# Kernel optimization log

Measured on AMD Instinct MI355X. Metric: run time of the kernel, lower is better.

The kernel has to match this reference:

```python
import jax, jax.numpy as jnp
import numpy as np
import math

N_EMB = 256
N_HEAD = 8
B_SEGS = 128
T_SEG = 256  # equal-length segments; N = B_SEGS * T_SEG


def setup_inputs() -> dict:
    key = jax.random.key(0)
    ks = jax.random.split(key, 10)
    N = B_SEGS * T_SEG
    x = jax.random.normal(ks[0], (N, N_EMB), dtype=jnp.float32)
    batch = jnp.repeat(jnp.arange(B_SEGS, dtype=jnp.int64), T_SEG)
    s = 1.0 / math.sqrt(N_EMB)
    def lin(k):
        kw, kb = jax.random.split(k)
        W = jax.random.uniform(kw, (N_EMB, N_EMB), jnp.float32, -s, s)
        b = jax.random.uniform(kb, (N_EMB,), jnp.float32, -s, s)
        return W, b
    Wq, bq = lin(ks[1])
    Wk, bk = lin(ks[2])
    Wv, bv = lin(ks[3])
    Wp, bp = lin(ks[4])
    return {"x": x, "batch": batch, "Wq": Wq, "bq": bq, "Wk": Wk, "bk": bk,
            "Wv": Wv, "bv": bv, "Wp": Wp, "bp": bp}


def reference(x, batch, Wq, bq, Wk, bk, Wv, bv, Wp, bp):
    # Dropout layers are identity in eval / p=0.
    N, C = x.shape
    H = N_HEAD
    hd = C // H
    B = int(batch[-1]) + 1        # equal-length segments
    T = N // B
    xr = x.reshape(B, T, C)
    # per-segment QKV projections: [B,H,T,hd]
    def heads(W, b):
        return (xr @ W.T + b).reshape(B, T, H, hd).transpose(0, 2, 1, 3)
    q = heads(Wq, bq)
    k = heads(Wk, bk)
    v = heads(Wv, bv)
    scores = jnp.einsum('bhtd,bhsd->bhts', q, k) * (1.0 / math.sqrt(hd))
    attn = jax.nn.softmax(scores, axis=-1)          # [B,H,T,T]
    y = jnp.einsum('bhts,bhsd->bhtd', attn, v)      # [B,H,T,hd]
    y = y.transpose(0, 2, 1, 3).reshape(B, T, C)
    y = y @ Wp.T + bp
    attn_mean = attn.mean(axis=1)                   # head-mean per segment [B,T,T]
    return y.reshape(N, C), attn_mean
```

## Files before the change

### kernel.cpp

```cpp
#include <hip/hip_runtime.h>
#include <hip/hip_bf16.h>
#include <stdint.h>

typedef unsigned short u16;
typedef __bf16 bf16_t;
typedef bf16_t bf16x8 __attribute__((ext_vector_type(8)));
typedef float f32x4 __attribute__((ext_vector_type(4)));

#define NTOK 32768
#define CEMB 256
#define NHEAD 8
#define HD 32
#define BSEG 128
#define TSEG 256

#define SCQ (0.17677669529663687f * 1.4426950408889634f)

static __device__ __forceinline__ bf16x8 ld16(const u16* p) {
  uint4 v = *reinterpret_cast<const uint4*>(p);
  return __builtin_bit_cast(bf16x8, v);
}
static __device__ __forceinline__ u16 f2b(float f) {
  return __builtin_bit_cast(u16, (bf16_t)f);
}
static __device__ __forceinline__ uint4 cvt8(float4 a, float4 b) {
  u16 o[8] = {f2b(a.x), f2b(a.y), f2b(a.z), f2b(a.w),
              f2b(b.x), f2b(b.y), f2b(b.z), f2b(b.w)};
  return *reinterpret_cast<const uint4*>(o);
}

typedef __attribute__((address_space(1))) const void GASV;
typedef __attribute__((address_space(3))) void LASV;
static __device__ __forceinline__ void stage16(const u16* g, u16* l) {
  __builtin_amdgcn_global_load_lds((GASV*)g, (LASV*)l, 16, 0, 0);
}

__global__ __launch_bounds__(1024, 4)
void k_qkv(const float* __restrict__ x,
           const float* __restrict__ Wq, const float* __restrict__ Wk,
           const float* __restrict__ Wv,
           const float* __restrict__ bq, const float* __restrict__ bk,
           const float* __restrict__ bv,
           u16* __restrict__ q_ws, u16* __restrict__ k_ws, u16* __restrict__ v_ws) {
  const int d = blockIdx.x;
  const int m_idx = (d & 7) * 32 + (d >> 3);
  const int m0 = m_idx * 128;
  const int tid = threadIdx.x;
  const int w = tid >> 6, l = tid & 63;
  const int lr = l & 15, lg = l >> 4;
  const int wrP = w >> 2, wcP = w & 3;

  extern __shared__ char lds[];
  char* bounce = lds + 131072;

  const int brow = tid >> 2;
  const int bcb = (tid & 3) * 2;
  float4 breg[2][4];
  auto BLOAD = [&](int bi, float4* r4) {
    const float* Wsel = (bi >> 2) == 0 ? Wq : ((bi >> 2) == 1 ? Wk : Wv);
    const float* s = Wsel + (size_t)brow * CEMB + (bi & 3) * 64 + bcb * 8;
    r4[0] = reinterpret_cast<const float4*>(s)[0];
    r4[1] = reinterpret_cast<const float4*>(s)[1];
    r4[2] = reinterpret_cast<const float4*>(s)[2];
    r4[3] = reinterpret_cast<const float4*>(s)[3];
  };
  auto BWRITE = [&](const float4* r4, int par) {
    char* Bs = lds + 65536 + par * 32768;
#pragma unroll
    for (int jj = 0; jj < 2; ++jj) {
      int byte = brow * 128 + (((bcb + jj) * 16) ^ ((brow & 7) << 4));
      *reinterpret_cast<uint4*>(Bs + byte) = cvt8(r4[jj * 2], r4[jj * 2 + 1]);
    }
  };

  BLOAD(0, breg[0]);
  {
    int row = tid >> 3, seg = tid & 7;
    const float* src = x + (size_t)(m0 + row) * CEMB + seg * 32;
#pragma unroll
    for (int j = 0; j < 4; ++j) {
      float4 a = reinterpret_cast<const float4*>(src)[2 * j];
      float4 b = reinterpret_cast<const float4*>(src)[2 * j + 1];
      int byte = row * 512 + ((seg * 64 + j * 16) ^ ((row & 7) << 4));
      *reinterpret_cast<uint4*>(lds + byte) = cvt8(a, b);
    }
  }
  BWRITE(breg[0], 0);
  BLOAD(1, breg[1]);
  __syncthreads();

#pragma unroll
  for (int mode = 0; mode < 3; ++mode) {
    f32x4 acc[2][4];
#pragma unroll
    for (int mf = 0; mf < 2; ++mf)
#pragma unroll
      for (int nf = 0; nf < 4; ++nf) {
        f32x4 z = {0.f, 0.f, 0.f, 0.f};
        acc[mf][nf] = z;
      }

#pragma unroll
    for (int kt = 0; kt < 4; ++kt) {
      const int bi = mode * 4 + kt;
      const int par = bi & 1;
      if (bi < 11) BWRITE(breg[(bi + 1) & 1], (bi + 1) & 1);
      if (bi < 10) BLOAD(bi + 2, breg[bi & 1]);
      const char* Bs = lds + 65536 + par * 32768;
      bf16x8 av[2][2], bw[4][2];
#pragma unroll
      for (int mf = 0; mf < 2; ++mf)
#pragma unroll
        for (int kk = 0; kk < 2; ++kk) {
          int row = wrP * 32 + mf * 16 + lr;
          int byte = row * 512 + ((kt * 128 + kk * 64 + lg * 16) ^ ((row & 7) << 4));
          av[mf][kk] = *reinterpret_cast<const bf16x8*>(lds + byte);
        }
#pragma unroll
      for (int nf = 0; nf < 4; ++nf)
#pragma unroll
        for (int kk = 0; kk < 2; ++kk) {
          int row = wcP * 64 + nf * 16 + lr;
          int byte = row * 128 + ((kk * 64 + lg * 16) ^ ((row & 7) << 4));
          bw[nf][kk] = *reinterpret_cast<const bf16x8*>(Bs + byte);
        }
#pragma unroll
      for (int kk = 0; kk < 2; ++kk)
#pragma unroll
        for (int nf = 0; nf < 4; ++nf)
#pragma unroll
          for (int mf = 0; mf < 2; ++mf)
            acc[mf][nf] = __builtin_amdgcn_mfma_f32_16x16x32_bf16(
                av[mf][kk], bw[nf][kk], acc[mf][nf], 0, 0, 0);
      __syncthreads();
    }

    const float* bias = (mode == 0) ? bq : ((mode == 1) ? bk : bv);
    float bb[4];
#pragma unroll
    for (int nf = 0; nf < 4; ++nf) bb[nf] = bias[wcP * 64 + nf * 16 + lr];

    if (mode < 2) {
      const float osc = (mode == 0) ? SCQ : 1.0f;
      u16* outp = (mode == 0) ? q_ws : k_ws;
#pragma unroll
      for (int g = 0; g < 2; ++g) {
        if ((wrP >> 1) == g) {
#pragma unroll
          for (int mf = 0; mf < 2; ++mf)
#pragma unroll
            for (int nf = 0; nf < 4; ++nf)
#pragma unroll
              for (int r = 0; r < 4; ++r) {
                int lrow = (wrP & 1) * 32 + mf * 16 + lg * 4 + r;
                int col = wcP * 64 + nf * 16 + lr;
                int byte = lrow * 512 + ((col * 2) ^ ((lrow & 7) << 4));
                *(u16*)(bounce + byte) = f2b((acc[mf][nf][r] + bb[nf]) * osc);
              }
        }
        __syncthreads();
#pragma unroll
        for (int jj = 0; jj < 2; ++jj) {
          int ch = tid * 2 + jj;
          int crow = ch >> 5, cc = ch & 31;
          int byte = crow * 512 + ((cc * 16) ^ ((crow & 7) << 4));
          *reinterpret_cast<uint4*>(outp + (size_t)(m0 + g * 64 + crow) * CEMB + cc * 8) =
              *reinterpret_cast<const uint4*>(bounce + byte);
        }
        __syncthreads();
      }
    } else {
      const int bs = m0 >> 8, t0 = m0 & 255;
#pragma unroll
      for (int g = 0; g < 2; ++g) {
        if ((wcP >> 1) == g) {
#pragma unroll
          for (int mf = 0; mf < 2; ++mf)
#pragma unroll
            for (int nf = 0; nf < 4; ++nf)
#pragma unroll
              for (int r = 0; r < 4; ++r) {
                int row = wrP * 32 + mf * 16 + lg * 4 + r;
                int ccol = (wcP & 1) * 64 + nf * 16 + lr;
                int byte = ccol * 256 + ((row * 2) ^ ((ccol & 7) << 4));
                *(u16*)(bounce + byte) = f2b(acc[mf][nf][r] + bb[nf]);
              }
        }
        __syncthreads();
#pragma unroll
        for (int jj = 0; jj < 2; ++jj) {
          int ch = tid * 2 + jj;
          int ccl = ch >> 4, cc = ch & 15;
          int byte = ccl * 256 + ((cc * 16) ^ ((ccl & 7) << 4));
          int c = g * 128 + ccl, hh = c >> 5, dd = c & 31;
          *reinterpret_cast<uint4*>(
              v_ws + ((size_t)(bs * NHEAD + hh) * HD + dd) * TSEG + t0 + cc * 8) =
              *reinterpret_cast<const uint4*>(bounce + byte);
        }
        __syncthreads();
      }
    }
  }
}

__global__ __launch_bounds__(1024, 4)
void k_attn(const u16* __restrict__ q_ws, const u16* __restrict__ k_ws,
            const u16* __restrict__ v_ws, const float* __restrict__ Wp,
            const float* __restrict__ bp,
            float* __restrict__ out, float* __restrict__ mean_out) {
  const int dblk = blockIdx.x;
  const int xcd = dblk & 7, ii = dblk >> 3;
  const int b = xcd * 16 + (ii >> 1);
  const int th = ii & 1;
  const int tid = threadIdx.x;
  const int w = tid >> 6, l = tid & 63;
  const int lr = l & 15, lg = l >> 4;
  const int wt = w & 7, sh = w >> 3;
  const int tbase = th * 128 + wt * 16;

  extern __shared__ u16 ldsKV[];
  float* smb = reinterpret_cast<float*>(ldsKV + 32768);
  float* ylds = reinterpret_cast<float*>(ldsKV + 33280);
  char* yTile = reinterpret_cast<char*>(ldsKV) + 83968;

  float macc[8][4];
#pragma unroll
  for (int st = 0; st < 8; ++st)
#pragma unroll
    for (int r = 0; r < 4; ++r) macc[st][r] = 0.f;

  const u16* qseg = q_ws + (size_t)b * TSEG * CEMB;
  const u16* kseg = k_ws + (size_t)b * TSEG * CEMB;
  const u16* vseg = v_ws + (size_t)(b * NHEAD) * HD * TSEG;

  auto STAGE_KV = [&](int hn, int bn) {
    int idx = tid;
    int c = idx >> 6, l2 = idx & 63;
    int lr2 = l2 & 15, lg2 = l2 >> 4;
    int srow = 32 * (c >> 1) + 4 * (c & 1) + 8 * (lr2 >> 2) + (lr2 & 3);
    stage16(kseg + srow * CEMB + hn * HD + lg2 * 8, ldsKV + (bn * 1024 + idx) * 8);
    int vrow = (c >> 3) * 16 + lr2;
    int vcol = (c & 7) * 32 + lg2 * 8;
    stage16(vseg + (size_t)(hn * HD + vrow) * TSEG + vcol,
            ldsKV + 16384 + (bn * 1024 + idx) * 8);
  };

  STAGE_KV(0, 0);
  bf16x8 qf = ld16(qseg + (tbase + lr) * CEMB + lg * 8);

  const int own_slot = wt * 2 + sh;
  const int par_slot = wt * 2 + (1 - sh);

  for (int h = 0; h < NHEAD; ++h) {
    const int bn = h & 1;
    __syncthreads();
    if (h < 7) STAGE_KV(h + 1, bn ^ 1);
    const u16* Kb = ldsKV + bn * 8192;
    const u16* Vb = ldsKV + 16384 + bn * 8192;

    float s[8][4];
    __builtin_amdgcn_s_setprio(1);
#pragma unroll
    for (int st = 0; st < 8; ++st) {
      bf16x8 kf = *reinterpret_cast<const bf16x8*>(Kb + ((sh * 8 + st) * 64 + l) * 8);
      f32x4 z = {0.f, 0.f, 0.f, 0.f};
      f32x4 dd = __builtin_amdgcn_mfma_f32_16x16x32_bf16(kf, qf, z, 0, 0, 0);
#pragma unroll
      for (int r = 0; r < 4; ++r) s[st][r] = dd[r];
    }
    __builtin_amdgcn_s_setprio(0);

    qf = ld16(qseg + (tbase + lr) * CEMB + ((h + 1) & 7) * HD + lg * 8);

    float s0 = 0.f, s1 = 0.f, s2 = 0.f, s3 = 0.f;
#pragma unroll
    for (int st = 0; st < 8; ++st) {
      float p0 = exp2f(s[st][0]);
      float p1 = exp2f(s[st][1]);
      float p2 = exp2f(s[st][2]);
      float p3 = exp2f(s[st][3]);
      s[st][0] = p0; s[st][1] = p1; s[st][2] = p2; s[st][3] = p3;
      s0 += p0; s1 += p1; s2 += p2; s3 += p3;
    }
    float sm = (s0 + s1) + (s2 + s3);
    sm += __shfl_xor(sm, 16, 64);
    sm += __shfl_xor(sm, 32, 64);

    bf16x8 pb[4];
#pragma unroll
    for (int kk = 0; kk < 4; ++kk)
#pragma unroll
      for (int e = 0; e < 4; ++e) {
        pb[kk][e] = (bf16_t)s[2 * kk][e];
        pb[kk][4 + e] = (bf16_t)s[2 * kk + 1][e];
      }

    f32x4 y0 = {0.f, 0.f, 0.f, 0.f}, y1 = {0.f, 0.f, 0.f, 0.f};
    __builtin_amdgcn_s_setprio(1);
#pragma unroll
    for (int kk = 0; kk < 4; ++kk) {
      bf16x8 vf0 = *reinterpret_cast<const bf16x8*>(Vb + ((0 * 8 + sh * 4 + kk) * 64 + l) * 8);
      bf16x8 vf1 = *reinterpret_cast<const bf16x8*>(Vb + ((1 * 8 + sh * 4 + kk) * 64 + l) * 8);
      y0 = __builtin_amdgcn_mfma_f32_16x16x32_bf16(vf0, pb[kk], y0, 0, 0, 0);
      y1 = __builtin_amdgcn_mfma_f32_16x16x32_bf16(vf1, pb[kk], y1, 0, 0, 0);
    }
    __builtin_amdgcn_s_setprio(0);

    if (l < 16) smb[own_slot * 16 + l] = sm;
    {
      f32x4 ywr = (sh == 0) ? y1 : y0;
      *reinterpret_cast<f32x4*>(ylds + own_slot * 272 + lg * 68 + lr * 4) = ywr;
    }

    __builtin_amdgcn_sched_barrier(0);
    asm volatile("s_waitcnt lgkmcnt(0)" ::: "memory");
    __builtin_amdgcn_s_barrier();
    __builtin_amdgcn_sched_barrier(0);

    float smT = sm + smb[par_slot * 16 + lr];
    float inv = __builtin_amdgcn_rcpf(smT);

#pragma unroll
    for (int st = 0; st < 8; ++st)
#pragma unroll
      for (int r = 0; r < 4; ++r)
        macc[st][r] = fmaf(s[st][r], inv, macc[st][r]);

    {
      f32x4 ymine = (sh == 0) ? y0 : y1;
      f32x4 ypar = *reinterpret_cast<const f32x4*>(ylds + par_slot * 272 + lg * 68 + lr * 4);
      u16 o[4];
#pragma unroll
      for (int r = 0; r < 4; ++r) o[r] = f2b((ymine[r] + ypar[r]) * inv);
      int row = wt * 16 + lr;
      int colb = h * 64 + sh * 32 + lg * 8;
      *reinterpret_cast<uint2*>(yTile + row * 512 + (colb ^ ((row & 7) << 4))) =
          *reinterpret_cast<const uint2*>(o);
    }
  }

  __syncthreads();

  const int wrow = tid >> 2;
  const int wcb = (tid & 3) * 2;
  float4 wreg[2][4];
  auto WLOAD = [&](int kt, float4* r4) {
    const float* s = Wp + (size_t)wrow * CEMB + kt * 64 + wcb * 8;
    r4[0] = reinterpret_cast<const float4*>(s)[0];
    r4[1] = reinterpret_cast<const float4*>(s)[1];
    r4[2] = reinterpret_cast<const float4*>(s)[2];
    r4[3] = reinterpret_cast<const float4*>(s)[3];
  };
  auto WWRITE = [&](const float4* r4, int bn) {
#pragma unroll
    for (int jj = 0; jj < 2; ++jj) {
      int byte = bn * 32768 + wrow * 128 + (((wcb + jj) * 16) ^ ((wrow & 7) << 4));
      *reinterpret_cast<uint4*>(reinterpret_cast<char*>(ldsKV) + byte) =
          cvt8(r4[jj * 2], r4[jj * 2 + 1]);
    }
  };

  WLOAD(0, wreg[0]);

  {
    float* smem = reinterpret_cast<float*>(ldsKV);
    float* smw = smem + w * (16 * 65) + lr * 65;
    const int trow = l >> 2;
    const int cql = (l & 3) * 4;
    const float* srcp = smem + w * (16 * 65) + trow * 65 + cql;
    float* gdst = mean_out + (size_t)(b * TSEG + tbase + trow) * TSEG + sh * 128 + cql;
    for (int c = 0; c < 2; ++c) {
#pragma unroll
      for (int j = 0; j < 4; ++j) {
        int st = 4 * c + j;
        int sl = 32 * ((st >> 1) & 1) + 4 * (st & 1) + 8 * lg;
#pragma unroll
        for (int r = 0; r < 4; ++r) smw[sl + r] = macc[st][r] * 0.125f;
      }
#pragma unroll
      for (int j = 0; j < 4; ++j)
        *reinterpret_cast<f32x4*>(gdst + c * 64 + j * 16) =
            *reinterpret_cast<const f32x4*>(srcp + j * 16);
    }
  }
  __syncthreads();

  {
    const int wrP = w >> 2, wcP = w & 3;

    WWRITE(wreg[0], 0);
    WLOAD(1, wreg[1]);
    __syncthreads();

    f32x4 acc[2][4];
#pragma unroll
    for (int mf = 0; mf < 2; ++mf)
#pragma unroll
      for (int nf = 0; nf < 4; ++nf) {
        f32x4 z = {0.f, 0.f, 0.f, 0.f};
        acc[mf][nf] = z;
      }

#pragma unroll
    for (int kt = 0; kt < 4; ++kt) {
      int buf = kt & 1;
      if (kt < 3) WWRITE(wreg[(kt + 1) & 1], buf ^ 1);
      if (kt < 2) WLOAD(kt + 2, wreg[kt & 1]);
      const char* Wb = reinterpret_cast<const char*>(ldsKV) + buf * 32768;
      bf16x8 av[2][2], bw[4][2];
#pragma unroll
      for (int mf = 0; mf < 2; ++mf)
#pragma unroll
        for (int kk = 0; kk < 2; ++kk) {
          int row = wrP * 32 + mf * 16 + lr;
          int byte = row * 512 + ((kt * 128 + kk * 64 + lg * 16) ^ ((row & 7) << 4));
          av[mf][kk] = *reinterpret_cast<const bf16x8*>(yTile + byte);
        }
#pragma unroll
      for (int nf = 0; nf < 4; ++nf)
#pragma unroll
        for (int kk = 0; kk < 2; ++kk) {
          int row = wcP * 64 + nf * 16 + lr;
          int byte = row * 128 + ((kk * 64 + lg * 16) ^ ((row & 7) << 4));
          bw[nf][kk] = *reinterpret_cast<const bf16x8*>(Wb + byte);
        }
#pragma unroll
      for (int kk = 0; kk < 2; ++kk)
#pragma unroll
        for (int nf = 0; nf < 4; ++nf)
#pragma unroll
          for (int mf = 0; mf < 2; ++mf)
            acc[mf][nf] = __builtin_amdgcn_mfma_f32_16x16x32_bf16(
                av[mf][kk], bw[nf][kk], acc[mf][nf], 0, 0, 0);
      __syncthreads();
    }

    float bb[4];
#pragma unroll
    for (int nf = 0; nf < 4; ++nf) bb[nf] = bp[wcP * 64 + nf * 16 + lr];
#pragma unroll
    for (int mf = 0; mf < 2; ++mf)
#pragma unroll
      for (int nf = 0; nf < 4; ++nf)
#pragma unroll
        for (int r = 0; r < 4; ++r) {
          int m = b * TSEG + th * 128 + wrP * 32 + mf * 16 + lg * 4 + r;
          int c = wcP * 64 + nf * 16 + lr;
          out[(size_t)m * CEMB + c] = acc[mf][nf][r] + bb[nf];
        }
  }
}

extern "C" void kernel_launch(void* const* d_in, const int* in_sizes, int n_in,
                              void* d_out, int out_size, void* d_ws, size_t ws_size,
                              hipStream_t stream) {
  (void)in_sizes; (void)n_in; (void)out_size; (void)ws_size;
  const float* x  = (const float*)d_in[0];
  const float* Wq = (const float*)d_in[2];
  const float* bq = (const float*)d_in[3];
  const float* Wk = (const float*)d_in[4];
  const float* bk = (const float*)d_in[5];
  const float* Wv = (const float*)d_in[6];
  const float* bv = (const float*)d_in[7];
  const float* Wp = (const float*)d_in[8];
  const float* bp = (const float*)d_in[9];
  float* out = (float*)d_out;

  char* ws = (char*)d_ws;
  u16* q_ws = (u16*)(ws);
  u16* k_ws = (u16*)(ws + 16777216);
  u16* v_ws = (u16*)(ws + 33554432);
  float* mean_out = out + (size_t)NTOK * CEMB;

  k_qkv<<<256, 1024, 163840, stream>>>(x, Wq, Wk, Wv, bq, bk, bv, q_ws, k_ws, v_ws);
  k_attn<<<256, 1024, 149504, stream>>>(q_ws, k_ws, v_ws, Wp, bp, out, mean_out);
}
```

Measured before the change: 90.43 us.

## Pre-convert weights to bf16 once and stage them into LDS asynchronously

Adds a small kernel that converts Wq, Wk, Wv and Wp to bf16 in workspace once per call. The QKV kernel then stages weight tiles directly into LDS with global_load_lds instead of doing register loads plus fp32-to-bf16 conversion, and the attention kernel loads bf16 Wp without converting it. This is meant to cut redundant per-block conversion work and halve weight read traffic. The cost is an extra launch and a little more global traffic, and the async staging relies on the existing barriers for ordering.

After: 91.23 us. Within noise of the previous version (+0.9%).

```diff
diff --git a/kernel.cpp b/kernel.cpp
--- a/kernel.cpp
+++ b/kernel.cpp
@@ -35,10 +35,20 @@
   __builtin_amdgcn_global_load_lds((GASV*)g, (LASV*)l, 16, 0, 0);
 }
 
+__global__ void k_convw(const float* __restrict__ wq, const float* __restrict__ wk,
+                        const float* __restrict__ wv, const float* __restrict__ wp,
+                        u16* __restrict__ wb) {
+  int slot = blockIdx.x * blockDim.x + threadIdx.x;
+  int wsel = slot >> 13;
+  int off = (slot & 8191) * 8;
+  const float* s0 = (wsel == 0) ? wq : ((wsel == 1) ? wk : ((wsel == 2) ? wv : wp));
+  float4 a = reinterpret_cast<const float4*>(s0 + off)[0];
+  float4 b = reinterpret_cast<const float4*>(s0 + off)[1];
+  *reinterpret_cast<uint4*>(wb + wsel * 65536 + off) = cvt8(a, b);
+}
+
 __global__ __launch_bounds__(1024, 4)
-void k_qkv(const float* __restrict__ x,
-           const float* __restrict__ Wq, const float* __restrict__ Wk,
-           const float* __restrict__ Wv,
+void k_qkv(const float* __restrict__ x, const u16* __restrict__ wb,
            const float* __restrict__ bq, const float* __restrict__ bk,
            const float* __restrict__ bv,
            u16* __restrict__ q_ws, u16* __restrict__ k_ws, u16* __restrict__ v_ws) {
@@ -53,27 +63,20 @@
   extern __shared__ char lds[];
   char* bounce = lds + 131072;
 
-  const int brow = tid >> 2;
-  const int bcb = (tid & 3) * 2;
-  float4 breg[2][4];
-  auto BLOAD = [&](int bi, float4* r4) {
-    const float* Wsel = (bi >> 2) == 0 ? Wq : ((bi >> 2) == 1 ? Wk : Wv);
-    const float* s = Wsel + (size_t)brow * CEMB + (bi & 3) * 64 + bcb * 8;
-    r4[0] = reinterpret_cast<const float4*>(s)[0];
-    r4[1] = reinterpret_cast<const float4*>(s)[1];
-    r4[2] = reinterpret_cast<const float4*>(s)[2];
-    r4[3] = reinterpret_cast<const float4*>(s)[3];
+  auto BSTAGE = [&](int bi, int par) {
+    const u16* W = wb + (bi >> 2) * 65536;
+    const int ktl = bi & 3;
+    u16* dstb = (u16*)(lds + 65536 + par * 32768);
+#pragma unroll
+    for (int r = 0; r < 2; ++r) {
+      int id = r * 1024 + tid;
+      int row = id >> 3, p = id & 7;
+      int scb = (p * 16) ^ ((row & 7) << 4);
+      stage16(W + (size_t)row * CEMB + ktl * 64 + (scb >> 1), dstb + id * 8);
+    }
   };
-  auto BWRITE = [&](const float4* r4, int par) {
-    char* Bs = lds + 65536 + par * 32768;
-#pragma unroll
-    for (int jj = 0; jj < 2; ++jj) {
-      int byte = brow * 128 + (((bcb + jj) * 16) ^ ((brow & 7) << 4));
-      *reinterpret_cast<uint4*>(Bs + byte) = cvt8(r4[jj * 2], r4[jj * 2 + 1]);
-    }
-  };
-
-  BLOAD(0, breg[0]);
+
+  BSTAGE(0, 0);
   {
     int row = tid >> 3, seg = tid & 7;
     const float* src = x + (size_t)(m0 + row) * CEMB + seg * 32;
@@ -85,8 +88,6 @@
       *reinterpret_cast<uint4*>(lds + byte) = cvt8(a, b);
     }
   }
-  BWRITE(breg[0], 0);
-  BLOAD(1, breg[1]);
   __syncthreads();
 
 #pragma unroll
@@ -104,8 +105,7 @@
     for (int kt = 0; kt < 4; ++kt) {
       const int bi = mode * 4 + kt;
       const int par = bi & 1;
-      if (bi < 11) BWRITE(breg[(bi + 1) & 1], (bi + 1) & 1);
-      if (bi < 10) BLOAD(bi + 2, breg[bi & 1]);
+      if (bi < 11) BSTAGE(bi + 1, par ^ 1);
       const char* Bs = lds + 65536 + par * 32768;
       bf16x8 av[2][2], bw[4][2];
 #pragma unroll
@@ -205,7 +205,7 @@
 
 __global__ __launch_bounds__(1024, 4)
 void k_attn(const u16* __restrict__ q_ws, const u16* __restrict__ k_ws,
-            const u16* __restrict__ v_ws, const float* __restrict__ Wp,
+            const u16* __restrict__ v_ws, const u16* __restrict__ wb,
             const float* __restrict__ bp,
             float* __restrict__ out, float* __restrict__ mean_out) {
   const int dblk = blockIdx.x;
@@ -343,20 +343,17 @@
 
   const int wrow = tid >> 2;
   const int wcb = (tid & 3) * 2;
-  float4 wreg[2][4];
-  auto WLOAD = [&](int kt, float4* r4) {
-    const float* s = Wp + (size_t)wrow * CEMB + kt * 64 + wcb * 8;
-    r4[0] = reinterpret_cast<const float4*>(s)[0];
-    r4[1] = reinterpret_cast<const float4*>(s)[1];
-    r4[2] = reinterpret_cast<const float4*>(s)[2];
-    r4[3] = reinterpret_cast<const float4*>(s)[3];
+  uint4 wreg[2][2];
+  auto WLOAD = [&](int kt, uint4* r4) {
+    const u16* s = wb + 3 * 65536 + (size_t)wrow * CEMB + kt * 64 + wcb * 8;
+    r4[0] = *reinterpret_cast<const uint4*>(s);
+    r4[1] = *reinterpret_cast<const uint4*>(s + 8);
   };
-  auto WWRITE = [&](const float4* r4, int bn) {
+  auto WWRITE = [&](const uint4* r4, int bn) {
 #pragma unroll
     for (int jj = 0; jj < 2; ++jj) {
       int byte = bn * 32768 + wrow * 128 + (((wcb + jj) * 16) ^ ((wrow & 7) << 4));
-      *reinterpret_cast<uint4*>(reinterpret_cast<char*>(ldsKV) + byte) =
-          cvt8(r4[jj * 2], r4[jj * 2 + 1]);
+      *reinterpret_cast<uint4*>(reinterpret_cast<char*>(ldsKV) + byte) = r4[jj];
     }
   };
 
@@ -470,8 +467,10 @@
   u16* q_ws = (u16*)(ws);
   u16* k_ws = (u16*)(ws + 16777216);
   u16* v_ws = (u16*)(ws + 33554432);
+  u16* wb   = (u16*)(ws + 50331648);
   float* mean_out = out + (size_t)NTOK * CEMB;
 
-  k_qkv<<<256, 1024, 163840, stream>>>(x, Wq, Wk, Wv, bq, bk, bv, q_ws, k_ws, v_ws);
-  k_attn<<<256, 1024, 149504, stream>>>(q_ws, k_ws, v_ws, Wp, bp, out, mean_out);
-}
+  k_convw<<<128, 256, 0, stream>>>(Wq, Wk, Wv, Wp, wb);
+  k_qkv<<<256, 1024, 163840, stream>>>(x, wb, bq, bk, bv, q_ws, k_ws, v_ws);
+  k_attn<<<256, 1024, 149504, stream>>>(q_ws, k_ws, v_ws, wb, bp, out, mean_out);
+}
```

## Defer softmax normalization by one head to remove per-head mid-loop barrier

Applied to the files above, without the earlier changes.

In the attention kernel, each wave half now writes its partner's partial PV output into the yTile as bf16 and double-buffers the row-sum exchange. Normalization and accumulation for head h-1 are deferred until after the next loop-top barrier, which removes the extra per-head s_barrier. In the QKV kernel, the B-tile write and prefetch are moved after the MFMAs, and launch bounds drop to one block per CU. The partial sums now pass through bf16 before being combined, which adds rounding error to y.

New measurement: 105.4 us. 1.17x slower.

```diff
diff --git a/kernel.cpp b/kernel.cpp
--- a/kernel.cpp
+++ b/kernel.cpp
@@ -23,6 +23,10 @@
 static __device__ __forceinline__ u16 f2b(float f) {
   return __builtin_bit_cast(u16, (bf16_t)f);
 }
+static __device__ __forceinline__ float b2f(u16 v) {
+  uint32_t u = ((uint32_t)v) << 16;
+  return __builtin_bit_cast(float, u);
+}
 static __device__ __forceinline__ uint4 cvt8(float4 a, float4 b) {
   u16 o[8] = {f2b(a.x), f2b(a.y), f2b(a.z), f2b(a.w),
               f2b(b.x), f2b(b.y), f2b(b.z), f2b(b.w)};
@@ -35,7 +39,7 @@
   __builtin_amdgcn_global_load_lds((GASV*)g, (LASV*)l, 16, 0, 0);
 }
 
-__global__ __launch_bounds__(1024, 4)
+__global__ __launch_bounds__(1024, 1)
 void k_qkv(const float* __restrict__ x,
            const float* __restrict__ Wq, const float* __restrict__ Wk,
            const float* __restrict__ Wv,
@@ -104,8 +108,6 @@
     for (int kt = 0; kt < 4; ++kt) {
       const int bi = mode * 4 + kt;
       const int par = bi & 1;
-      if (bi < 11) BWRITE(breg[(bi + 1) & 1], (bi + 1) & 1);
-      if (bi < 10) BLOAD(bi + 2, breg[bi & 1]);
       const char* Bs = lds + 65536 + par * 32768;
       bf16x8 av[2][2], bw[4][2];
 #pragma unroll
@@ -132,6 +134,8 @@
           for (int mf = 0; mf < 2; ++mf)
             acc[mf][nf] = __builtin_amdgcn_mfma_f32_16x16x32_bf16(
                 av[mf][kk], bw[nf][kk], acc[mf][nf], 0, 0, 0);
+      if (bi < 11) BWRITE(breg[(bi + 1) & 1], par ^ 1);
+      if (bi < 10) BLOAD(bi + 2, breg[bi & 1]);
       __syncthreads();
     }
 
@@ -203,7 +207,7 @@
   }
 }
 
-__global__ __launch_bounds__(1024, 4)
+__global__ __launch_bounds__(1024, 1)
 void k_attn(const u16* __restrict__ q_ws, const u16* __restrict__ k_ws,
             const u16* __restrict__ v_ws, const float* __restrict__ Wp,
             const float* __restrict__ bp,
@@ -220,7 +224,6 @@
 
   extern __shared__ u16 ldsKV[];
   float* smb = reinterpret_cast<float*>(ldsKV + 32768);
-  float* ylds = reinterpret_cast<float*>(ldsKV + 33280);
   char* yTile = reinterpret_cast<char*>(ldsKV) + 83968;
 
   float macc[8][4];
@@ -250,15 +253,40 @@
 
   const int own_slot = wt * 2 + sh;
   const int par_slot = wt * 2 + (1 - sh);
+  const int yrow = wt * 16 + lr;
+
+  float s[8][4];
+  float sm = 0.f;
+  f32x4 ymine = {0.f, 0.f, 0.f, 0.f};
 
   for (int h = 0; h < NHEAD; ++h) {
     const int bn = h & 1;
     __syncthreads();
     if (h < 7) STAGE_KV(h + 1, bn ^ 1);
+
+    if (h > 0) {
+      const int hp = h - 1;
+      float smT = sm + smb[(hp & 1) * 256 + par_slot * 16 + lr];
+      float inv = __builtin_amdgcn_rcpf(smT);
+#pragma unroll
+      for (int st = 0; st < 8; ++st)
+#pragma unroll
+        for (int r = 0; r < 4; ++r)
+          macc[st][r] = fmaf(s[st][r], inv, macc[st][r]);
+      int colb = hp * 64 + sh * 32 + lg * 8;
+      char* yp = yTile + yrow * 512 + (colb ^ ((yrow & 7) << 4));
+      uint2 part = *reinterpret_cast<const uint2*>(yp);
+      const u16* pw = reinterpret_cast<const u16*>(&part);
+      u16 o[4];
+#pragma unroll
+      for (int r = 0; r < 4; ++r)
+        o[r] = f2b((ymine[r] + b2f(pw[r])) * inv);
+      *reinterpret_cast<uint2*>(yp) = *reinterpret_cast<const uint2*>(o);
+    }
+
     const u16* Kb = ldsKV + bn * 8192;
     const u16* Vb = ldsKV + 16384 + bn * 8192;
 
-    float s[8][4];
     __builtin_amdgcn_s_setprio(1);
 #pragma unroll
     for (int st = 0; st < 8; ++st) {
@@ -282,7 +310,7 @@
       s[st][0] = p0; s[st][1] = p1; s[st][2] = p2; s[st][3] = p3;
       s0 += p0; s1 += p1; s2 += p2; s3 += p3;
     }
-    float sm = (s0 + s1) + (s2 + s3);
+    sm = (s0 + s1) + (s2 + s3);
     sm += __shfl_xor(sm, 16, 64);
     sm += __shfl_xor(sm, 32, 64);
 
@@ -306,50 +334,48 @@
     }
     __builtin_amdgcn_s_setprio(0);
 
-    if (l < 16) smb[own_slot * 16 + l] = sm;
+    if (l < 16) smb[(h & 1) * 256 + own_slot * 16 + l] = sm;
     {
-      f32x4 ywr = (sh == 0) ? y1 : y0;
-      *reinterpret_cast<f32x4*>(ylds + own_slot * 272 + lg * 68 + lr * 4) = ywr;
-    }
-
-    __builtin_amdgcn_sched_barrier(0);
-    asm volatile("s_waitcnt lgkmcnt(0)" ::: "memory");
-    __builtin_amdgcn_s_barrier();
-    __builtin_amdgcn_sched_barrier(0);
-
-    float smT = sm + smb[par_slot * 16 + lr];
+      f32x4 yo = (sh == 0) ? y1 : y0;
+      int colb = h * 64 + (1 - sh) * 32 + lg * 8;
+      u16 o[4] = {f2b(yo[0]), f2b(yo[1]), f2b(yo[2]), f2b(yo[3])};
+      *reinterpret_cast<uint2*>(yTile + yrow * 512 + (colb ^ ((yrow & 7) << 4))) =
+          *reinterpret_cast<const uint2*>(o);
+    }
+    ymine = (sh == 0) ? y0 : y1;
+  }
+
+  __syncthreads();
+
+  {
+    const int hp = 7;
+    float smT = sm + smb[(hp & 1) * 256 + par_slot * 16 + lr];
     float inv = __builtin_amdgcn_rcpf(smT);
-
 #pragma unroll
     for (int st = 0; st < 8; ++st)
 #pragma unroll
       for (int r = 0; r < 4; ++r)
         macc[st][r] = fmaf(s[st][r], inv, macc[st][r]);
-
-    {
-      f32x4 ymine = (sh == 0) ? y0 : y1;
-      f32x4 ypar = *reinterpret_cast<const f32x4*>(ylds + par_slot * 272 + lg * 68 + lr * 4);
-      u16 o[4];
-#pragma unroll
-      for (int r = 0; r < 4; ++r) o[r] = f2b((ymine[r] + ypar[r]) * inv);
-      int row = wt * 16 + lr;
-      int colb = h * 64 + sh * 32 + lg * 8;
-      *reinterpret_cast<uint2*>(yTile + row * 512 + (colb ^ ((row & 7) << 4))) =
-          *reinterpret_cast<const uint2*>(o);
-    }
+    int colb = hp * 64 + sh * 32 + lg * 8;
+    char* yp = yTile + yrow * 512 + (colb ^ ((yrow & 7) << 4));
+    uint2 part = *reinterpret_cast<const uint2*>(yp);
+    const u16* pw = reinterpret_cast<const u16*>(&part);
+    u16 o[4];
+#pragma unroll
+    for (int r = 0; r < 4; ++r)
+      o[r] = f2b((ymine[r] + b2f(pw[r])) * inv);
+    *reinterpret_cast<uint2*>(yp) = *reinterpret_cast<const uint2*>(o);
   }
-
-  __syncthreads();
 
   const int wrow = tid >> 2;
   const int wcb = (tid & 3) * 2;
   float4 wreg[2][4];
   auto WLOAD = [&](int kt, float4* r4) {
-    const float* s = Wp + (size_t)wrow * CEMB + kt * 64 + wcb * 8;
-    r4[0] = reinterpret_cast<const float4*>(s)[0];
-    r4[1] = reinterpret_cast<const float4*>(s)[1];
-    r4[2] = reinterpret_cast<const float4*>(s)[2];
-    r4[3] = reinterpret_cast<const float4*>(s)[3];
+    const float* s2 = Wp + (size_t)wrow * CEMB + kt * 64 + wcb * 8;
+    r4[0] = reinterpret_cast<const float4*>(s2)[0];
+    r4[1] = reinterpret_cast<const float4*>(s2)[1];
+    r4[2] = reinterpret_cast<const float4*>(s2)[2];
+    r4[3] = reinterpret_cast<const float4*>(s2)[3];
   };
   auto WWRITE = [&](const float4* r4, int bn) {
 #pragma unroll
```
